# Performance work log

Measured on AMD Instinct MI355X. Metric: run time of the kernel, lower is better.

Reference implementation:

```python
import jax, jax.numpy as jnp
import numpy as np

DG = 8   # deformable groups
K = 3    # DCNv2 kernel size


def conv1x1(x, w):
    return jnp.einsum('bhwc,cf->bhwf', x, w)


def conv3x3_same(x, w, b):
    out = jax.lax.conv_general_dilated(x, w, (1, 1), 'SAME',
                                       dimension_numbers=('NHWC', 'HWIO', 'NHWC'))
    return out + b


def dcn_v2(x, offset, mask, weight, bias):
    # x: [B,H,W,C]; offset: [B,H,W,DG,K*K,2] (dy,dx); mask: [B,H,W,DG,K*K]
    B, H, W, C = x.shape
    cpg = C // DG
    ky, kx = jnp.meshgrid(jnp.arange(K) - (K // 2), jnp.arange(K) - (K // 2), indexing='ij')
    ky = ky.reshape(-1).astype(x.dtype)  # [K*K]
    kx = kx.reshape(-1).astype(x.dtype)
    iy = jnp.arange(H, dtype=x.dtype)[None, :, None, None, None]
    ix = jnp.arange(W, dtype=x.dtype)[None, None, :, None, None]
    yp = iy + ky + offset[..., 0]   # [B,H,W,DG,KK] sample rows
    xp = ix + kx + offset[..., 1]   # sample cols

    # group-major flattened feature map for gather: [B,DG,H*W,cpg]
    xt = jnp.transpose(x.reshape(B, H, W, DG, cpg), (0, 3, 1, 2, 4)).reshape(B, DG, H * W, cpg)

    def gather(yi, xi):
        valid = ((yi >= 0) & (yi < H) & (xi >= 0) & (xi < W)).astype(x.dtype)
        yc = jnp.clip(yi, 0, H - 1)
        xc = jnp.clip(xi, 0, W - 1)
        flat = (yc * W + xc).astype(jnp.int32)               # [B,H,W,DG,KK]
        idx = jnp.transpose(flat, (0, 3, 1, 2, 4)).reshape(B, DG, -1)
        v = jnp.take_along_axis(xt, idx[..., None], axis=2)  # [B,DG,H*W*KK,cpg]
        v = v.reshape(B, DG, H, W, K * K, cpg)
        v = jnp.transpose(v, (0, 2, 3, 1, 4, 5))             # [B,H,W,DG,KK,cpg]
        return v * valid[..., None]

    y0 = jnp.floor(yp); x0 = jnp.floor(xp)
    wy = (yp - y0)[..., None]; wx = (xp - x0)[..., None]
    val = (gather(y0, x0) * (1 - wy) * (1 - wx)
           + gather(y0, x0 + 1) * (1 - wy) * wx
           + gather(y0 + 1, x0) * wy * (1 - wx)
           + gather(y0 + 1, x0 + 1) * wy * wx)
    val = val * mask[..., None]                               # modulated sampling
    # [B,H,W,DG,KK,cpg] -> [B,H,W,KK,C] (global channel = g*cpg + r)
    val = jnp.transpose(val, (0, 1, 2, 4, 3, 5)).reshape(B, H, W, K * K, C)
    out = jnp.einsum('bhwkc,kcf->bhwf', val, weight.reshape(K * K, C, -1))
    return out + bias


def setup_inputs() -> dict:
    key = jax.random.key(0)
    ks = jax.random.split(key, 8)
    B, H, W, Cf, Cc, F = 4, 64, 64, 256, 256, 256
    fine = jax.random.normal(ks[0], (B, H, W, Cf), jnp.float32)
    coarse = jax.random.normal(ks[1], (B, H // 2, W // 2, Cc), jnp.float32)
    attend_w = jax.random.normal(ks[2], (Cf, Cf), jnp.float32) * 0.05
    select_w = jax.random.normal(ks[3], (Cf, F), jnp.float32) * 0.05
    offset_w = jax.random.normal(ks[4], (F + Cc, 2 * F), jnp.float32) * 0.05
    om_w = jax.random.normal(ks[5], (3, 3, 2 * F, DG * 3 * K * K), jnp.float32) * 0.01
    om_b = jnp.zeros((DG * 3 * K * K,), jnp.float32)
    dcn_w = jax.random.normal(ks[6], (3, 3, Cc, F), jnp.float32) * 0.05
    dcn_b = jnp.zeros((F,), jnp.float32)
    return {'fine': fine, 'coarse': coarse, 'attend_w': attend_w, 'select_w': select_w,
            'offset_w': offset_w, 'om_w': om_w, 'om_b': om_b, 'dcn_w': dcn_w, 'dcn_b': dcn_b}


def reference(fine, coarse, attend_w, select_w, offset_w, om_w, om_b, dcn_w, dcn_b):
    B, H, W, Cf = fine.shape
    Cc = coarse.shape[-1]
    # BilinearInterpolation: upsample coarse to fine resolution
    coarse_up = jax.image.resize(coarse, (B, H, W, Cc), 'bilinear')
    # FeatureSelection: GAP -> 1x1 sigmoid attention, residual gate, 1x1 proj
    attn = jax.nn.sigmoid(conv1x1(jnp.mean(fine, axis=(1, 2), keepdims=True), attend_w))
    fine_cal = conv1x1(fine * (attn + 1.0), select_w)
    # offset features from concat(selected fine, 2*coarse)
    align = conv1x1(jnp.concatenate([fine_cal, coarse_up * 2.0], axis=-1), offset_w)
    # DCNv2 internal offset/mask conv (3x3) on alignment features
    om = conv3x3_same(align, om_w, om_b)          # [B,H,W,DG*3*K*K]
    n_off = DG * 2 * K * K
    off = om[..., :n_off].reshape(B, H, W, DG, K * K, 2)
    mask = jax.nn.sigmoid(om[..., n_off:]).reshape(B, H, W, DG, K * K)
    aligned = dcn_v2(coarse_up, off, mask, dcn_w, dcn_b)
    return jax.nn.relu(aligned) + fine_cal
```

## Files before the change

### kernel.cpp

```cpp
#include <hip/hip_runtime.h>
#include <math.h>


typedef __attribute__((ext_vector_type(8))) short bf16x8;
typedef __attribute__((ext_vector_type(4))) short bf16x4;
typedef __attribute__((ext_vector_type(4))) float f32x4;
#define MFMA16(a,b,c) __builtin_amdgcn_mfma_f32_16x16x32_bf16(a,b,c,0,0,0)

__device__ inline short f2b(float x){
  union { float f; unsigned u; } v; v.f = x;
  unsigned r = v.u + 0x7FFFu + ((v.u >> 16) & 1u);
  return (short)(r >> 16);
}
__device__ inline float b2f(short s){
  union { unsigned u; float f; } v;
  v.u = ((unsigned)(unsigned short)s) << 16;
  return v.f;
}

#define OFS_GATE  1024u
#define OFS_PART  2048u
#define OFS_CUPB  264192u
#define OFS_FCAL  4458496u
#define OFS_ALGB  8652800u
#define OFS_OM    12847104u
#define OFS_DWB   16386048u
#define OFS_OMWB  16680960u
#define OFS_SWB   17270784u
#define OFS_OWB   17401856u

__global__ __launch_bounds__(256) void k_gap(const float* __restrict__ fine,
                                             float* __restrict__ part){
  __shared__ float red[4*256];
  int b = blockIdx.x >> 6, chunk = blockIdx.x & 63;
  int c4 = threadIdx.x & 63, rl = threadIdx.x >> 6;
  const float4* F4 = (const float4*)fine;
  float4 s = {0.f,0.f,0.f,0.f};
  for (int it = 0; it < 16; ++it){
    int row = chunk*64 + it*4 + rl;
    float4 v = F4[((size_t)(b*4096 + row))*64 + c4];
    s.x += v.x; s.y += v.y; s.z += v.z; s.w += v.w;
  }
  *(float4*)&red[rl*256 + c4*4] = s;
  __syncthreads();
  int c = threadIdx.x;
  part[(size_t)blockIdx.x*256 + c] = red[c] + red[256+c] + red[512+c] + red[768+c];
}

__global__ __launch_bounds__(256) void k_misc(const float* __restrict__ part,
                                              const float* __restrict__ aw,
                                              float* __restrict__ gate,
                                              const float* __restrict__ dw,
                                              const float* __restrict__ omw,
                                              const float* __restrict__ ow,
                                              const float* __restrict__ sw,
                                              short* __restrict__ dwb,
                                              short* __restrict__ omwb,
                                              short* __restrict__ owb,
                                              short* __restrict__ swb,
                                              const float* __restrict__ coarse,
                                              short* __restrict__ cupb){
  int blk = blockIdx.x;
  if (blk < 4){
    __shared__ float m[256];
    int b = blk, f = threadIdx.x;
    float t0 = 0.f, t1 = 0.f, t2 = 0.f, t3 = 0.f;
#pragma unroll 4
    for (int ch = 0; ch < 64; ch += 4){
      t0 += part[(size_t)(b*64 + ch    )*256 + f];
      t1 += part[(size_t)(b*64 + ch + 1)*256 + f];
      t2 += part[(size_t)(b*64 + ch + 2)*256 + f];
      t3 += part[(size_t)(b*64 + ch + 3)*256 + f];
    }
    m[f] = ((t0 + t1) + (t2 + t3)) * (1.f/4096.f);
    __syncthreads();
    float s0 = 0.f, s1 = 0.f, s2 = 0.f, s3 = 0.f;
#pragma unroll 4
    for (int c = 0; c < 256; c += 4){
      s0 += m[c    ] * aw[(c    )*256 + f];
      s1 += m[c + 1] * aw[(c + 1)*256 + f];
      s2 += m[c + 2] * aw[(c + 2)*256 + f];
      s3 += m[c + 3] * aw[(c + 3)*256 + f];
    }
    float s = (s0 + s1) + (s2 + s3);
    gate[b*256 + f] = 1.f + 1.f/(1.f + expf(-s));
  } else if (blk < 292){
    int t = (blk - 4)*256 + threadIdx.x;
    int l = t & 63, nt = (t >> 6) & 15, ksg = t >> 10;
    int n = nt*16 + (l & 15);
    int kb = ksg*32 + (l >> 4)*8;
    bf16x8 o;
#pragma unroll
    for (int j = 0; j < 8; ++j) o[j] = f2b(dw[(size_t)(kb + j)*256 + n]);
    ((bf16x8*)dwb)[t] = o;
  } else if (blk < 868){
    int t = (blk - 292)*256 + threadIdx.x;
    int l = t & 63, nt = (t >> 6) & 15, ksg = t >> 10;
    int n = nt*16 + (l & 15);
    int kb = ksg*32 + (l >> 4)*8;
    bf16x8 o;
#pragma unroll
    for (int j = 0; j < 8; ++j)
      o[j] = (n < 216) ? f2b(omw[(size_t)(kb + j)*216 + n]) : (short)0;
    ((bf16x8*)omwb)[t] = o;
  } else if (blk < 996){
    int t = (blk - 868)*256 + threadIdx.x;
    int l = t & 63, nt = (t >> 6) & 31, ksg = t >> 11;
    int n = nt*16 + (l & 15);
    int kb = ksg*32 + (l >> 4)*8;
    float sc = (kb >= 256) ? 2.f : 1.f;
    bf16x8 o;
#pragma unroll
    for (int j = 0; j < 8; ++j) o[j] = f2b(sc * ow[(size_t)(kb + j)*512 + n]);
    ((bf16x8*)owb)[t] = o;
  } else if (blk < 1124){
    int t = (blk - 996)*256 + threadIdx.x;
    int l = t & 63, nt = (t >> 6) & 15, ksg = t >> 10;
    int n = nt*16 + (l & 15);
    int kb = ksg*32 + (l >> 4)*8;
    bf16x8 o;
#pragma unroll
    for (int j = 0; j < 8; ++j) o[j] = f2b(sw[(size_t)(kb + j)*256 + n]);
    ((bf16x8*)swb)[t] = o;
  } else {
    int idx = (blk - 1124)*256 + threadIdx.x;
    int c4 = idx & 63, x = (idx >> 6) & 63, y = (idx >> 12) & 63, b = idx >> 18;
    float fy = 0.5f*y - 0.25f, fx = 0.5f*x - 0.25f;
    float yf = floorf(fy), xf = floorf(fx);
    float wy = fy - yf, wx = fx - xf;
    int r0 = max(0, min(31, (int)yf)), r1 = max(0, min(31, (int)yf + 1));
    int c0 = max(0, min(31, (int)xf)), c1 = max(0, min(31, (int)xf + 1));
    const float4* src = (const float4*)coarse;
    float4 v00 = src[((b*32 + r0)*32 + c0)*64 + c4];
    float4 v01 = src[((b*32 + r0)*32 + c1)*64 + c4];
    float4 v10 = src[((b*32 + r1)*32 + c0)*64 + c4];
    float4 v11 = src[((b*32 + r1)*32 + c1)*64 + c4];
    float w00 = (1.f-wy)*(1.f-wx), w01 = (1.f-wy)*wx, w10 = wy*(1.f-wx), w11 = wy*wx;
    bf16x4 o = { f2b(v00.x*w00 + v01.x*w01 + v10.x*w10 + v11.x*w11),
                 f2b(v00.y*w00 + v01.y*w01 + v10.y*w10 + v11.y*w11),
                 f2b(v00.z*w00 + v01.z*w01 + v10.z*w10 + v11.z*w11),
                 f2b(v00.w*w00 + v01.w*w01 + v10.w*w10 + v11.w*w11) };
    ((bf16x4*)cupb)[idx] = o;
  }
}

#define FST 264
__global__ __launch_bounds__(512) void k_fa(const float* __restrict__ fine,
                                            const float* __restrict__ gate,
                                            const short* __restrict__ swb,
                                            const short* __restrict__ owb,
                                            const short* __restrict__ cupb,
                                            float* __restrict__ fcal,
                                            short* __restrict__ algb){
  __shared__ float g4[256];
  __shared__ short ab[32*FST];
  int bid = ((blockIdx.x & 7) << 6) | (blockIdx.x >> 3);
  int m0 = bid*32, b = m0 >> 12;
  int tid = threadIdx.x, lane = tid & 63, wave = tid >> 6;
  int arow = lane & 15, aquad = lane >> 4;
  if (tid < 256) g4[tid] = gate[b*256 + tid];
  __syncthreads();
  const float4* F4 = (const float4*)(fine + (size_t)m0*256);
  const float4* G4 = (const float4*)g4;
  for (int it = 0; it < 4; ++it){
    int idx = it*512 + tid;
    int row = idx >> 6, c4 = idx & 63;
    float4 v = F4[row*64 + c4];
    float4 gg = G4[c4];
    bf16x4 s4 = { f2b(v.x*gg.x), f2b(v.y*gg.y), f2b(v.z*gg.z), f2b(v.w*gg.w) };
    *(bf16x4*)&ab[row*FST + c4*4] = s4;
  }
  __syncthreads();
  f32x4 acc[2][2];
#pragma unroll
  for (int s = 0; s < 2; ++s)
#pragma unroll
    for (int t = 0; t < 2; ++t) acc[s][t] = (f32x4){0.f,0.f,0.f,0.f};
  const bf16x8* W8 = (const bf16x8*)swb;
  for (int ks = 0; ks < 8; ++ks){
    bf16x8 a0 = *(const bf16x8*)&ab[arow*FST + ks*32 + aquad*8];
    bf16x8 a1 = *(const bf16x8*)&ab[(16 + arow)*FST + ks*32 + aquad*8];
    const bf16x8* wp = W8 + ((size_t)(ks*16 + wave*2))*64 + lane;
#pragma unroll
    for (int t = 0; t < 2; ++t){
      bf16x8 bw = wp[t*64];
      acc[0][t] = MFMA16(a0, bw, acc[0][t]);
      acc[1][t] = MFMA16(a1, bw, acc[1][t]);
    }
  }
  __syncthreads();
#pragma unroll
  for (int t = 0; t < 2; ++t){
    int f = wave*32 + t*16 + arow;
#pragma unroll
    for (int s = 0; s < 2; ++s)
#pragma unroll
      for (int r = 0; r < 4; ++r){
        int mloc = s*16 + aquad*4 + r;
        float v = acc[s][t][r];
        fcal[(size_t)(m0 + mloc)*256 + f] = v;
        ab[mloc*FST + f] = f2b(v);
      }
  }
  __syncthreads();
  f32x4 acc2[2][4];
#pragma unroll
  for (int s = 0; s < 2; ++s)
#pragma unroll
    for (int t = 0; t < 4; ++t) acc2[s][t] = (f32x4){0.f,0.f,0.f,0.f};
  const bf16x8* OW8 = (const bf16x8*)owb;
  for (int ks = 0; ks < 16; ++ks){
    bf16x8 a0, a1;
    if (ks < 8){
      a0 = *(const bf16x8*)&ab[arow*FST + ks*32 + aquad*8];
      a1 = *(const bf16x8*)&ab[(16 + arow)*FST + ks*32 + aquad*8];
    } else {
      int ko = (ks - 8)*32 + aquad*8;
      a0 = *(const bf16x8*)(cupb + (size_t)(m0 + arow)*256 + ko);
      a1 = *(const bf16x8*)(cupb + (size_t)(m0 + 16 + arow)*256 + ko);
    }
    const bf16x8* wp = OW8 + ((size_t)(ks*32 + wave*4))*64 + lane;
#pragma unroll
    for (int t = 0; t < 4; ++t){
      bf16x8 bw = wp[t*64];
      acc2[0][t] = MFMA16(a0, bw, acc2[0][t]);
      acc2[1][t] = MFMA16(a1, bw, acc2[1][t]);
    }
  }
#pragma unroll
  for (int t = 0; t < 4; ++t){
    int n = wave*64 + t*16 + arow;
#pragma unroll
    for (int s = 0; s < 2; ++s)
#pragma unroll
      for (int r = 0; r < 4; ++r){
        int m = m0 + s*16 + aquad*4 + r;
        algb[(size_t)m*512 + n] = f2b(acc2[s][t][r]);
      }
  }
}

#define XST2 264
__global__ __launch_bounds__(512) void k_om(const short* __restrict__ algb,
                                            const short* __restrict__ omwb,
                                            const float* __restrict__ omb,
                                            float* __restrict__ om){
  __shared__ short xbuf[66*XST2];
  int blk = ((blockIdx.x & 7) << 5) | (blockIdx.x >> 3);
  int m0 = blk*64;
  int b = m0 >> 12, y = (m0 >> 6) & 63;
  int tid = threadIdx.x;
  int lane = tid & 63, wave = tid >> 6;
  int arow = lane & 15, aquad = lane >> 4;
  f32x4 acc[4][2];
#pragma unroll
  for (int mi = 0; mi < 4; ++mi)
#pragma unroll
    for (int t = 0; t < 2; ++t) acc[mi][t] = (f32x4){0.f,0.f,0.f,0.f};
  const bf16x8* W8 = (const bf16x8*)omwb;
  for (int ky = 0; ky < 3; ++ky){
    int yy = y + ky - 1;
    if ((unsigned)yy >= 64u) continue;
    const short* srow = algb + (size_t)((b*64 + yy)*64)*512;
    for (int h = 0; h < 2; ++h){
      __syncthreads();
      for (int it = 0; it < 5; ++it){
        int u = it*512 + tid;
        if (u < 2112){
          int xx = u >> 5, cu = u & 31;
          int gx = xx - 1;
          bf16x8 v = (bf16x8){0,0,0,0,0,0,0,0};
          if ((unsigned)gx < 64u)
            v = *(const bf16x8*)(srow + (size_t)gx*512 + h*256 + cu*8);
          *(bf16x8*)&xbuf[xx*XST2 + cu*8] = v;
        }
      }
      __syncthreads();
#pragma unroll
      for (int kx = 0; kx < 3; ++kx){
        const bf16x8* wb = W8 + ((size_t)((ky*48 + kx*16 + h*8)*16 + wave*2))*64 + lane;
        bf16x8 c0 = wb[0], c1 = wb[64];
        for (int s = 0; s < 8; ++s){
          bf16x8 a[4];
#pragma unroll
          for (int mi = 0; mi < 4; ++mi)
            a[mi] = *(const bf16x8*)&xbuf[(mi*16 + arow + kx)*XST2 + s*32 + aquad*8];
          bf16x8 n0, n1;
          if (s < 7){ n0 = wb[(s+1)*1024]; n1 = wb[(s+1)*1024 + 64]; }
#pragma unroll
          for (int mi = 0; mi < 4; ++mi) acc[mi][0] = MFMA16(a[mi], c0, acc[mi][0]);
#pragma unroll
          for (int mi = 0; mi < 4; ++mi) acc[mi][1] = MFMA16(a[mi], c1, acc[mi][1]);
          if (s < 7){ c0 = n0; c1 = n1; }
        }
      }
    }
  }
#pragma unroll
  for (int t = 0; t < 2; ++t){
    int f = wave*32 + t*16 + arow;
    if (f < 216){
      float bias = omb[f];
      bool is_mask = (f >= 144);
#pragma unroll
      for (int mi = 0; mi < 4; ++mi)
#pragma unroll
        for (int r = 0; r < 4; ++r){
          int m = m0 + mi*16 + aquad*4 + r;
          float v = acc[mi][t][r] + bias;
          if (is_mask) v = 1.f/(1.f + expf(-v));
          om[(size_t)m*216 + f] = v;
        }
    }
  }
}

#define VST 776
__global__ __launch_bounds__(512, 4) void k_dcn(const short* __restrict__ cupb,
                                                const float* __restrict__ om,
                                                const short* __restrict__ dwb,
                                                const float* __restrict__ db,
                                                const float* __restrict__ fcal,
                                                float* __restrict__ out){
  __shared__ short valb[32*VST];
  int bid = ((blockIdx.x & 7) << 6) | (blockIdx.x >> 3);
  int m0 = bid*32;
  int b = m0 >> 12, y = (m0 & 4095) >> 6, x0 = m0 & 63;
  int tid = threadIdx.x;
  int lane = tid & 63, wave = tid >> 6;
  int unit = tid >> 2, lane4 = tid & 3;
  int arow = lane & 15, aquad = lane >> 4;
  f32x4 acc[2][2];
#pragma unroll
  for (int s = 0; s < 2; ++s)
#pragma unroll
    for (int t = 0; t < 2; ++t) acc[s][t] = (f32x4){0.f,0.f,0.f,0.f};
  const short* cpb = cupb + (size_t)b*4096*256;
  const bf16x8* W8 = (const bf16x8*)dwb;

  for (int ph = 0; ph < 3; ++ph){
    __syncthreads();
    bf16x8 L0[2], L1[2], L2[2], L3[2];
    float pwA[2], pwB[2], pwC[2], pwD[2], pmv[2];
    int pdst[2];
#define DCN_STAGE(S, IT)                                                     \
    {                                                                        \
      int u = (IT)*128 + unit;                                               \
      int i = u / 24; int r = u - i*24; int g = r / 3; int kk = r - g*3;     \
      const float* omp = om + (size_t)(m0 + i)*216;                          \
      int k = ph*3 + kk;                                                     \
      float dy = omp[(g*9 + k)*2 + 0];                                       \
      float dx = omp[(g*9 + k)*2 + 1];                                       \
      float mv = omp[144 + g*9 + k];                                         \
      float yp = (float)(y + ph - 1) + dy;                                   \
      float xp = (float)(x0 + i + kk - 1) + dx;                              \
      float yf = floorf(yp), xf = floorf(xp);                                \
      float wy = yp - yf, wx = xp - xf;                                      \
      int iy = (int)yf, ix = (int)xf;                                        \
      float wA = (1.f-wy)*(1.f-wx), wB = (1.f-wy)*wx;                        \
      float wC = wy*(1.f-wx), wD = wy*wx;                                    \
      bool y0ok = (unsigned)iy < 64u, y1ok = (unsigned)(iy+1) < 64u;         \
      bool x0ok = (unsigned)ix < 64u, x1ok = (unsigned)(ix+1) < 64u;         \
      if (!(y0ok && x0ok)) wA = 0.f;                                         \
      if (!(y0ok && x1ok)) wB = 0.f;                                         \
      if (!(y1ok && x0ok)) wC = 0.f;                                         \
      if (!(y1ok && x1ok)) wD = 0.f;                                         \
      int y0c = min(max(iy, 0), 63), y1c = min(max(iy + 1, 0), 63);          \
      int x0c = min(max(ix, 0), 63), x1c = min(max(ix + 1, 0), 63);          \
      int cofs = g*32 + lane4*8;                                             \
      L0[S] = *(const bf16x8*)(cpb + (size_t)(y0c*64 + x0c)*256 + cofs);     \
      L1[S] = *(const bf16x8*)(cpb + (size_t)(y0c*64 + x1c)*256 + cofs);     \
      L2[S] = *(const bf16x8*)(cpb + (size_t)(y1c*64 + x0c)*256 + cofs);     \
      L3[S] = *(const bf16x8*)(cpb + (size_t)(y1c*64 + x1c)*256 + cofs);     \
      pwA[S] = wA; pwB[S] = wB; pwC[S] = wC; pwD[S] = wD; pmv[S] = mv;       \
      pdst[S] = i*VST + kk*256 + g*32 + lane4*8;                             \
    }
    DCN_STAGE(0, 0)
#pragma unroll
    for (int it = 0; it < 6; ++it){
      int c = it & 1, nx = c ^ 1;
      if (it < 5){ DCN_STAGE(nx, it + 1) }
      bf16x8 o;
#pragma unroll
      for (int j = 0; j < 8; ++j){
        float v = pwA[c]*b2f(L0[c][j]) + pwB[c]*b2f(L1[c][j])
                + pwC[c]*b2f(L2[c][j]) + pwD[c]*b2f(L3[c][j]);
        o[j] = f2b(v * pmv[c]);
      }
      *(bf16x8*)&valb[pdst[c]] = o;
    }
#undef DCN_STAGE
    __syncthreads();
    const bf16x8* wb = W8 + ((size_t)((ph*24)*16 + wave*2))*64 + lane;
    bf16x8 c0 = wb[0], c1 = wb[64];
    for (int ks = 0; ks < 24; ++ks){
      bf16x8 a0 = *(const bf16x8*)&valb[arow*VST + ks*32 + aquad*8];
      bf16x8 a1 = *(const bf16x8*)&valb[(16 + arow)*VST + ks*32 + aquad*8];
      bf16x8 n0, n1;
      if (ks < 23){ n0 = wb[(ks+1)*1024]; n1 = wb[(ks+1)*1024 + 64]; }
      acc[0][0] = MFMA16(a0, c0, acc[0][0]);
      acc[1][0] = MFMA16(a1, c0, acc[1][0]);
      acc[0][1] = MFMA16(a0, c1, acc[0][1]);
      acc[1][1] = MFMA16(a1, c1, acc[1][1]);
      if (ks < 23){ c0 = n0; c1 = n1; }
    }
  }
#pragma unroll
  for (int t = 0; t < 2; ++t){
    int f = wave*32 + t*16 + (lane & 15);
    float bias = db[f];
#pragma unroll
    for (int s = 0; s < 2; ++s)
#pragma unroll
      for (int r = 0; r < 4; ++r){
        int m = m0 + s*16 + aquad*4 + r;
        out[(size_t)m*256 + f] = fmaxf(acc[s][t][r] + bias, 0.f) + fcal[(size_t)m*256 + f];
      }
  }
}

extern "C" void kernel_launch(void* const* d_in, const int* in_sizes, int n_in,
                              void* d_out, int out_size, void* d_ws, size_t ws_size,
                              hipStream_t stream){
  const float* fine     = (const float*)d_in[0];
  const float* coarse   = (const float*)d_in[1];
  const float* attend_w = (const float*)d_in[2];
  const float* select_w = (const float*)d_in[3];
  const float* offset_w = (const float*)d_in[4];
  const float* om_w     = (const float*)d_in[5];
  const float* om_b     = (const float*)d_in[6];
  const float* dcn_w    = (const float*)d_in[7];
  const float* dcn_b    = (const float*)d_in[8];
  float* out = (float*)d_out;
  float* ws  = (float*)d_ws;

  float* gate = ws + OFS_GATE;
  float* part = ws + OFS_PART;
  short* cupb = (short*)(ws + OFS_CUPB);
  float* fcal = ws + OFS_FCAL;
  short* algb = (short*)(ws + OFS_ALGB);
  float* om   = ws + OFS_OM;
  short* dwb  = (short*)(ws + OFS_DWB);
  short* omwb = (short*)(ws + OFS_OMWB);
  short* swb  = (short*)(ws + OFS_SWB);
  short* owb  = (short*)(ws + OFS_OWB);

  hipLaunchKernelGGL(k_gap,  dim3(256),  dim3(256), 0, stream, fine, part);
  hipLaunchKernelGGL(k_misc, dim3(5220), dim3(256), 0, stream, part, attend_w, gate,
                     dcn_w, om_w, offset_w, select_w, dwb, omwb, owb, swb, coarse, cupb);
  hipLaunchKernelGGL(k_fa,   dim3(512),  dim3(512), 0, stream, fine, gate, swb, owb,
                     cupb, fcal, algb);
  hipLaunchKernelGGL(k_om,   dim3(256),  dim3(512), 0, stream, algb, omwb, om_b, om);
  hipLaunchKernelGGL(k_dcn,  dim3(512),  dim3(512), 0, stream, cupb, om, dwb, dcn_b, fcal, out);
  (void)in_sizes; (void)n_in; (void)out_size; (void)ws_size;
}
```

Measured before the change: 217.6 us.

## Fuse offset/mask 3x3 conv into DCN kernel, keeping offsets in LDS

```diff
diff --git a/kernel.cpp b/kernel.cpp
--- a/kernel.cpp
+++ b/kernel.cpp
@@ -240,89 +240,21 @@
   }
 }
 
-#define XST2 264
-__global__ __launch_bounds__(512) void k_om(const short* __restrict__ algb,
-                                            const short* __restrict__ omwb,
-                                            const float* __restrict__ omb,
-                                            float* __restrict__ om){
-  __shared__ short xbuf[66*XST2];
-  int blk = ((blockIdx.x & 7) << 5) | (blockIdx.x >> 3);
-  int m0 = blk*64;
-  int b = m0 >> 12, y = (m0 >> 6) & 63;
-  int tid = threadIdx.x;
-  int lane = tid & 63, wave = tid >> 6;
-  int arow = lane & 15, aquad = lane >> 4;
-  f32x4 acc[4][2];
-#pragma unroll
-  for (int mi = 0; mi < 4; ++mi)
-#pragma unroll
-    for (int t = 0; t < 2; ++t) acc[mi][t] = (f32x4){0.f,0.f,0.f,0.f};
-  const bf16x8* W8 = (const bf16x8*)omwb;
-  for (int ky = 0; ky < 3; ++ky){
-    int yy = y + ky - 1;
-    if ((unsigned)yy >= 64u) continue;
-    const short* srow = algb + (size_t)((b*64 + yy)*64)*512;
-    for (int h = 0; h < 2; ++h){
-      __syncthreads();
-      for (int it = 0; it < 5; ++it){
-        int u = it*512 + tid;
-        if (u < 2112){
-          int xx = u >> 5, cu = u & 31;
-          int gx = xx - 1;
-          bf16x8 v = (bf16x8){0,0,0,0,0,0,0,0};
-          if ((unsigned)gx < 64u)
-            v = *(const bf16x8*)(srow + (size_t)gx*512 + h*256 + cu*8);
-          *(bf16x8*)&xbuf[xx*XST2 + cu*8] = v;
-        }
-      }
-      __syncthreads();
-#pragma unroll
-      for (int kx = 0; kx < 3; ++kx){
-        const bf16x8* wb = W8 + ((size_t)((ky*48 + kx*16 + h*8)*16 + wave*2))*64 + lane;
-        bf16x8 c0 = wb[0], c1 = wb[64];
-        for (int s = 0; s < 8; ++s){
-          bf16x8 a[4];
-#pragma unroll
-          for (int mi = 0; mi < 4; ++mi)
-            a[mi] = *(const bf16x8*)&xbuf[(mi*16 + arow + kx)*XST2 + s*32 + aquad*8];
-          bf16x8 n0, n1;
-          if (s < 7){ n0 = wb[(s+1)*1024]; n1 = wb[(s+1)*1024 + 64]; }
-#pragma unroll
-          for (int mi = 0; mi < 4; ++mi) acc[mi][0] = MFMA16(a[mi], c0, acc[mi][0]);
-#pragma unroll
-          for (int mi = 0; mi < 4; ++mi) acc[mi][1] = MFMA16(a[mi], c1, acc[mi][1]);
-          if (s < 7){ c0 = n0; c1 = n1; }
-        }
-      }
-    }
-  }
-#pragma unroll
-  for (int t = 0; t < 2; ++t){
-    int f = wave*32 + t*16 + arow;
-    if (f < 216){
-      float bias = omb[f];
-      bool is_mask = (f >= 144);
-#pragma unroll
-      for (int mi = 0; mi < 4; ++mi)
-#pragma unroll
-        for (int r = 0; r < 4; ++r){
-          int m = m0 + mi*16 + aquad*4 + r;
-          float v = acc[mi][t][r] + bias;
-          if (is_mask) v = 1.f/(1.f + expf(-v));
-          om[(size_t)m*216 + f] = v;
-        }
-    }
-  }
-}
-
+#define XOM 264
 #define VST 776
-__global__ __launch_bounds__(512, 4) void k_dcn(const short* __restrict__ cupb,
-                                                const float* __restrict__ om,
-                                                const short* __restrict__ dwb,
-                                                const float* __restrict__ db,
-                                                const float* __restrict__ fcal,
-                                                float* __restrict__ out){
-  __shared__ short valb[32*VST];
+#define OMS 216
+__global__ __launch_bounds__(512, 4) void k_omdcn(const short* __restrict__ algb,
+                                                  const short* __restrict__ omwb,
+                                                  const float* __restrict__ omb,
+                                                  const short* __restrict__ cupb,
+                                                  const short* __restrict__ dwb,
+                                                  const float* __restrict__ db,
+                                                  const float* __restrict__ fcal,
+                                                  float* __restrict__ out){
+  __shared__ __align__(16) char smem[77312];
+  short* xbuf = (short*)smem;
+  short* valb = (short*)smem;
+  float* om_s = (float*)(smem + 49664);
   int bid = ((blockIdx.x & 7) << 6) | (blockIdx.x >> 3);
   int m0 = bid*32;
   int b = m0 >> 12, y = (m0 & 4095) >> 6, x0 = m0 & 63;
@@ -330,6 +262,69 @@
   int lane = tid & 63, wave = tid >> 6;
   int unit = tid >> 2, lane4 = tid & 3;
   int arow = lane & 15, aquad = lane >> 4;
+
+  {
+    f32x4 acc[2][2];
+#pragma unroll
+    for (int mi = 0; mi < 2; ++mi)
+#pragma unroll
+      for (int t = 0; t < 2; ++t) acc[mi][t] = (f32x4){0.f,0.f,0.f,0.f};
+    const bf16x8* W8 = (const bf16x8*)omwb;
+    for (int ky = 0; ky < 3; ++ky){
+      int yy = y + ky - 1;
+      if ((unsigned)yy >= 64u) continue;
+      const short* srow = algb + (size_t)((b*64 + yy)*64)*512;
+      for (int h = 0; h < 2; ++h){
+        __syncthreads();
+        for (int it = 0; it < 3; ++it){
+          int u = it*512 + tid;
+          if (u < 1088){
+            int xx = u >> 5, cu = u & 31;
+            int gx = x0 - 1 + xx;
+            bf16x8 v = (bf16x8){0,0,0,0,0,0,0,0};
+            if ((unsigned)gx < 64u)
+              v = *(const bf16x8*)(srow + (size_t)gx*512 + h*256 + cu*8);
+            *(bf16x8*)&xbuf[xx*XOM + cu*8] = v;
+          }
+        }
+        __syncthreads();
+#pragma unroll
+        for (int kx = 0; kx < 3; ++kx){
+          const bf16x8* wb = W8 + ((size_t)((ky*48 + kx*16 + h*8)*16 + wave*2))*64 + lane;
+          bf16x8 c0 = wb[0], c1 = wb[64];
+          for (int s = 0; s < 8; ++s){
+            bf16x8 a0 = *(const bf16x8*)&xbuf[(arow + kx)*XOM + s*32 + aquad*8];
+            bf16x8 a1 = *(const bf16x8*)&xbuf[(16 + arow + kx)*XOM + s*32 + aquad*8];
+            bf16x8 n0, n1;
+            if (s < 7){ n0 = wb[(s+1)*1024]; n1 = wb[(s+1)*1024 + 64]; }
+            acc[0][0] = MFMA16(a0, c0, acc[0][0]);
+            acc[1][0] = MFMA16(a1, c0, acc[1][0]);
+            acc[0][1] = MFMA16(a0, c1, acc[0][1]);
+            acc[1][1] = MFMA16(a1, c1, acc[1][1]);
+            if (s < 7){ c0 = n0; c1 = n1; }
+          }
+        }
+      }
+    }
+#pragma unroll
+    for (int t = 0; t < 2; ++t){
+      int f = wave*32 + t*16 + arow;
+      if (f < 216){
+        float bias = omb[f];
+        bool is_mask = (f >= 144);
+#pragma unroll
+        for (int mi = 0; mi < 2; ++mi)
+#pragma unroll
+          for (int r = 0; r < 4; ++r){
+            int mloc = mi*16 + aquad*4 + r;
+            float v = acc[mi][t][r] + bias;
+            if (is_mask) v = 1.f/(1.f + expf(-v));
+            om_s[mloc*OMS + f] = v;
+          }
+      }
+    }
+  }
+
   f32x4 acc[2][2];
 #pragma unroll
   for (int s = 0; s < 2; ++s)
@@ -347,7 +342,7 @@
     {                                                                        \
       int u = (IT)*128 + unit;                                               \
       int i = u / 24; int r = u - i*24; int g = r / 3; int kk = r - g*3;     \
-      const float* omp = om + (size_t)(m0 + i)*216;                          \
+      const float* omp = om_s + i*OMS;                                       \
       int k = ph*3 + kk;                                                     \
       float dy = omp[(g*9 + k)*2 + 0];                                       \
       float dx = omp[(g*9 + k)*2 + 1];                                       \
@@ -439,7 +434,6 @@
   short* cupb = (short*)(ws + OFS_CUPB);
   float* fcal = ws + OFS_FCAL;
   short* algb = (short*)(ws + OFS_ALGB);
-  float* om   = ws + OFS_OM;
   short* dwb  = (short*)(ws + OFS_DWB);
   short* omwb = (short*)(ws + OFS_OMWB);
   short* swb  = (short*)(ws + OFS_SWB);
@@ -450,7 +444,7 @@
                      dcn_w, om_w, offset_w, select_w, dwb, omwb, owb, swb, coarse, cupb);
   hipLaunchKernelGGL(k_fa,   dim3(512),  dim3(512), 0, stream, fine, gate, swb, owb,
                      cupb, fcal, algb);
-  hipLaunchKernelGGL(k_om,   dim3(256),  dim3(512), 0, stream, algb, omwb, om_b, om);
-  hipLaunchKernelGGL(k_dcn,  dim3(512),  dim3(512), 0, stream, cupb, om, dwb, dcn_b, fcal, out);
+  hipLaunchKernelGGL(k_omdcn, dim3(512), dim3(512), 0, stream, algb, omwb, om_b,
+                     cupb, dwb, dcn_b, fcal, out);
   (void)in_sizes; (void)n_in; (void)out_size; (void)ws_size;
 }
```

After: 207.6 us. 1.05x faster.
